# Optimization experiments

Hardware: AMD Instinct MI355X
Metric: run time of the kernel (lower is better)

The kernel has to match this reference:

```python
import jax, jax.numpy as jnp
import numpy as np

N, Q, D = 512, 1024, 256  # num_nodes(=batch), query_len(context len), input_dim


def setup_inputs() -> dict:
    key = jax.random.key(0)
    ks = jax.random.split(key, 7)
    return {
        "query": jax.random.normal(ks[0], (N, 1, D), dtype=jnp.float32),
        "context": jax.random.normal(ks[1], (N, Q, D), dtype=jnp.float32),
        # torch nn.Linear weights are [out_features, in_features]
        "W_in": jax.random.normal(ks[2], (D, D), dtype=jnp.float32) / np.sqrt(D).astype(np.float32),
        "W_out": jax.random.normal(ks[3], (D, 2 * D), dtype=jnp.float32) / np.sqrt(2 * D).astype(np.float32),
        # per-node decay params [num_nodes,1,1]; positive so exp(-ab*dt) decays
        "ae": jax.random.uniform(ks[4], (N, 1, 1), dtype=jnp.float32),
        "ad": jax.random.uniform(ks[5], (N, 1, 1), dtype=jnp.float32),
        "ab": jax.random.uniform(ks[6], (N, 1, 1), dtype=jnp.float32),
        "index": 0,  # stored on self in the original, unused in forward math
    }


def reference(query, context, W_in, W_out, ae, ad, ab, index):
    # general attention: project query
    q = query @ W_in.T                                   # [N,1,D]
    scores = jnp.einsum('bod,bqd->boq', q, context)      # [N,1,Q]
    attention_weights = jax.nn.softmax(scores, axis=-1)  # [N,1,Q]
    ctx_t = jnp.swapaxes(context, 1, 2)                  # [N,D,Q]
    mix = attention_weights * ctx_t                      # [N,D,Q]  (broadcast over D)
    # delta_t = flip(arange(Q)) = [Q-1, ..., 0]
    delta_t = jnp.arange(Q - 1, -1, -1, dtype=jnp.float32)[None, None, :]  # [1,1,Q]
    bt = jnp.exp(-ab * delta_t)                          # [N,1,Q]
    mb = mix * bt                                        # [N,D,Q]
    term_2 = jnp.abs(ae * mb)
    term_3 = jnp.abs(ad * mb)  # |-ad * mix * bt| == |ad * mix * bt|
    mix2 = jnp.tanh(jnp.sum(term_2 + mix - term_3, axis=-1))[:, None, :]  # [N,1,D]
    combined = jnp.concatenate([mix2, q], axis=2)        # [N,1,2D]
    output = jnp.tanh(combined @ W_out.T)                # [N,1,D]
    return output, attention_weights
```

## Files before the change

### kernel.cpp

```cpp
#include <hip/hip_runtime.h>
#include <math.h>

#define N_NODES 512
#define QLEN    1024
#define DIM     256
#define TJ      16
#define LROW    264
#define NT      (QLEN / TJ)

#define AS1 __attribute__((address_space(1)))
#define AS3 __attribute__((address_space(3)))
#define GLD16(gsrc, ldst) \
  __builtin_amdgcn_global_load_lds((AS1 const void*)(gsrc), (AS3 void*)(ldst), 16, 0, 0)

__global__ __launch_bounds__(256, 2) void attn_main_kernel(
    const float* __restrict__ query,
    const float* __restrict__ context,
    const float* __restrict__ W_in,
    const float* __restrict__ ae,
    const float* __restrict__ ad,
    const float* __restrict__ ab,
    float* __restrict__ scores_out,
    float* __restrict__ q_ws,
    float* __restrict__ mix2_ws,
    float* __restrict__ ml_ws)
{
  __shared__ float qs[DIM];
  __shared__ float qv[DIM];
  __shared__ float sc_all[QLEN];
  __shared__ float tile[2][TJ * LROW];

  const int b    = blockIdx.x;
  const int tid  = threadIdx.x;
  const int wave = tid >> 6;
  const int lane = tid & 63;
  const int grp  = tid >> 4;
  const int gl   = tid & 15;

  const float* ctx = context + (size_t)b * QLEN * DIM;

  qs[tid] = query[b * DIM + tid];
  __syncthreads();

  #pragma unroll
  for (int i = 0; i < 4; ++i) {
    const int r = wave + i * 4;
    GLD16(ctx + (size_t)r * DIM + lane * 4, &tile[0][r * LROW]);
  }

  float acc = 0.f;
  {
    const float4* w4 = (const float4*)(W_in + (size_t)tid * DIM);
    #pragma unroll 8
    for (int k = 0; k < DIM / 4; ++k) {
      const float4 wv = w4[k];
      acc += wv.x * qs[4 * k] + wv.y * qs[4 * k + 1] +
             wv.z * qs[4 * k + 2] + wv.w * qs[4 * k + 3];
    }
  }
  qv[tid] = acc;
  q_ws[b * DIM + tid] = acc;

  const float ab_v = ab[b];

  float m = -INFINITY;
  float l = 0.f;
  float accA = 0.f;
  float accB = 0.f;

  for (int t = 0; t < NT; ++t) {
    const int cur = t & 1;

    __syncthreads();

    if (t + 1 < NT) {
      const float* src = ctx + (size_t)(t + 1) * TJ * DIM;
      #pragma unroll
      for (int i = 0; i < 4; ++i) {
        const int r = wave + i * 4;
        GLD16(src + (size_t)r * DIM + lane * 4, &tile[cur ^ 1][r * LROW]);
      }
    }

    {
      const float* trow = &tile[cur][grp * LROW];
      float p = 0.f;
      #pragma unroll
      for (int k = 0; k < TJ; ++k) {
        const int d = gl + 16 * k;
        p += trow[d] * qv[d];
      }
      p += __shfl_xor(p, 1);
      p += __shfl_xor(p, 2);
      p += __shfl_xor(p, 4);
      p += __shfl_xor(p, 8);
      if (gl == 0) sc_all[t * TJ + grp] = p;
    }

    asm volatile("s_waitcnt lgkmcnt(0)\n\ts_barrier" ::: "memory");

    {
      const float* sct = &sc_all[t * TJ];
      float tm = m;
      #pragma unroll
      for (int j = 0; j < TJ; ++j) tm = fmaxf(tm, sct[j]);
      const float rsc = __expf(m - tm);
      m = tm;
      l    *= rsc;
      accA *= rsc;
      accB *= rsc;
      const float* tb  = &tile[cur][tid];
      const float  dt0 = (float)(QLEN - 1 - t * TJ);
      #pragma unroll
      for (int j = 0; j < TJ; ++j) {
        const float w   = __expf(sct[j] - m);
        l += w;
        const float cv  = tb[j * LROW];
        const float btj = __expf(-ab_v * (dt0 - (float)j));
        accA += w * cv;
        accB += w * btj * fabsf(cv);
      }
    }
  }

  const float inv_l = 1.f / l;
  const float cb    = fabsf(ae[b]) - fabsf(ad[b]);
  mix2_ws[b * DIM + tid] = tanhf(accA * inv_l + cb * (accB * inv_l));
  if (tid == 0) { ml_ws[2 * b] = m; ml_ws[2 * b + 1] = l; }

  __syncthreads();
  #pragma unroll
  for (int c = 0; c < 4; ++c)
    scores_out[(size_t)b * QLEN + c * 256 + tid] = sc_all[c * 256 + tid];
}

__global__ __launch_bounds__(256) void out_gemm_kernel(
    const float* __restrict__ W_out,
    const float* __restrict__ q_ws,
    const float* __restrict__ mix2_ws,
    float* __restrict__ out)
{
  __shared__ float comb[2 * DIM];
  const int b = blockIdx.x, tid = threadIdx.x;
  comb[tid]       = mix2_ws[b * DIM + tid];
  comb[DIM + tid] = q_ws[b * DIM + tid];
  __syncthreads();

  const float4* w4 = (const float4*)(W_out + (size_t)tid * 2 * DIM);
  float acc = 0.f;
  #pragma unroll 8
  for (int k = 0; k < (2 * DIM) / 4; ++k) {
    const float4 wv = w4[k];
    acc += wv.x * comb[4 * k] + wv.y * comb[4 * k + 1] +
           wv.z * comb[4 * k + 2] + wv.w * comb[4 * k + 3];
  }
  out[(size_t)b * DIM + tid] = tanhf(acc);
}

__global__ __launch_bounds__(256) void attn_norm_kernel(
    float* __restrict__ scores, const float* __restrict__ ml)
{
  const int i = blockIdx.x * blockDim.x + threadIdx.x;
  const int b = i >> 10;
  const float m = ml[2 * b], l = ml[2 * b + 1];
  scores[i] = __expf(scores[i] - m) / l;
}

extern "C" void kernel_launch(void* const* d_in, const int* in_sizes, int n_in,
                              void* d_out, int out_size, void* d_ws, size_t ws_size,
                              hipStream_t stream) {
  const float* query   = (const float*)d_in[0];
  const float* context = (const float*)d_in[1];
  const float* W_in    = (const float*)d_in[2];
  const float* W_out   = (const float*)d_in[3];
  const float* ae      = (const float*)d_in[4];
  const float* ad      = (const float*)d_in[5];
  const float* ab      = (const float*)d_in[6];

  float* out        = (float*)d_out;
  float* scores_out = (float*)d_out + N_NODES * DIM;

  float* q_ws    = (float*)d_ws;
  float* mix2_ws = q_ws + N_NODES * DIM;
  float* ml_ws   = mix2_ws + N_NODES * DIM;

  hipLaunchKernelGGL(attn_main_kernel, dim3(N_NODES), dim3(256), 0, stream,
                     query, context, W_in, ae, ad, ab,
                     scores_out, q_ws, mix2_ws, ml_ws);
  hipLaunchKernelGGL(out_gemm_kernel, dim3(N_NODES), dim3(256), 0, stream,
                     W_out, q_ws, mix2_ws, out);
  hipLaunchKernelGGL(attn_norm_kernel, dim3((N_NODES * QLEN) / 256), dim3(256), 0, stream,
                     scores_out, ml_ws);
}
```

Measured before the change: 745.9 us.

## Fuse attention, output GEMM and normalization into one barrier-free wave-local kernel

```diff
diff --git a/kernel.cpp b/kernel.cpp
--- a/kernel.cpp
+++ b/kernel.cpp
@@ -7,163 +7,185 @@
 #define TJ      16
 #define LROW    264
 #define NT      (QLEN / TJ)
+#define NBUF    3
 
 #define AS1 __attribute__((address_space(1)))
 #define AS3 __attribute__((address_space(3)))
 #define GLD16(gsrc, ldst) \
   __builtin_amdgcn_global_load_lds((AS1 const void*)(gsrc), (AS3 void*)(ldst), 16, 0, 0)
 
-__global__ __launch_bounds__(256, 2) void attn_main_kernel(
+__global__ __launch_bounds__(256, 2) void rpps_fused_kernel(
     const float* __restrict__ query,
     const float* __restrict__ context,
     const float* __restrict__ W_in,
+    const float* __restrict__ W_out,
     const float* __restrict__ ae,
     const float* __restrict__ ad,
     const float* __restrict__ ab,
-    float* __restrict__ scores_out,
-    float* __restrict__ q_ws,
-    float* __restrict__ mix2_ws,
-    float* __restrict__ ml_ws)
+    float* __restrict__ out,
+    float* __restrict__ scores_out)
 {
   __shared__ float qs[DIM];
   __shared__ float qv[DIM];
-  __shared__ float sc_all[QLEN];
-  __shared__ float tile[2][TJ * LROW];
+  __shared__ float sc[QLEN];
+  __shared__ float comb[2 * DIM];
+  __shared__ float redM[4], redL[4];
+  __shared__ float redA[4][DIM], redB[4][DIM];
+  __shared__ float tile[NBUF][TJ * LROW];
 
   const int b    = blockIdx.x;
   const int tid  = threadIdx.x;
   const int wave = tid >> 6;
   const int lane = tid & 63;
-  const int grp  = tid >> 4;
+  const int wg   = (tid >> 4) & 3;
   const int gl   = tid & 15;
+  const int row  = 4 * wave + wg;
 
   const float* ctx = context + (size_t)b * QLEN * DIM;
 
   qs[tid] = query[b * DIM + tid];
-  __syncthreads();
-
-  #pragma unroll
-  for (int i = 0; i < 4; ++i) {
-    const int r = wave + i * 4;
-    GLD16(ctx + (size_t)r * DIM + lane * 4, &tile[0][r * LROW]);
-  }
-
-  float acc = 0.f;
+
+  #pragma unroll
+  for (int i = 0; i < 4; ++i)
+    GLD16(ctx + (size_t)(4 * wave + i) * DIM + lane * 4,
+          &tile[0][(4 * wave + i) * LROW]);
+  #pragma unroll
+  for (int i = 0; i < 4; ++i)
+    GLD16(ctx + (size_t)(TJ + 4 * wave + i) * DIM + lane * 4,
+          &tile[1][(4 * wave + i) * LROW]);
+
+  asm volatile("s_waitcnt lgkmcnt(0)\n\ts_barrier" ::: "memory");
+
+  float qp = 0.f;
   {
     const float4* w4 = (const float4*)(W_in + (size_t)tid * DIM);
     #pragma unroll 8
     for (int k = 0; k < DIM / 4; ++k) {
       const float4 wv = w4[k];
-      acc += wv.x * qs[4 * k] + wv.y * qs[4 * k + 1] +
-             wv.z * qs[4 * k + 2] + wv.w * qs[4 * k + 3];
-    }
-  }
-  qv[tid] = acc;
-  q_ws[b * DIM + tid] = acc;
+      qp += wv.x * qs[4 * k] + wv.y * qs[4 * k + 1] +
+            wv.z * qs[4 * k + 2] + wv.w * qs[4 * k + 3];
+    }
+  }
+  qv[tid] = qp;
+  asm volatile("s_waitcnt lgkmcnt(0)\n\ts_barrier" ::: "memory");
+
+  float qreg[16];
+  #pragma unroll
+  for (int k = 0; k < 16; ++k) qreg[k] = qv[gl + 16 * k];
 
   const float ab_v = ab[b];
-
-  float m = -INFINITY;
-  float l = 0.f;
-  float accA = 0.f;
-  float accB = 0.f;
-
+  float m_w = -INFINITY, l_w = 0.f;
+  float accA[16], accB[16];
+  #pragma unroll
+  for (int k = 0; k < 16; ++k) { accA[k] = 0.f; accB[k] = 0.f; }
+
+  int slot_c = 0, slot_p = 2;
   for (int t = 0; t < NT; ++t) {
-    const int cur = t & 1;
-
-    __syncthreads();
-
-    if (t + 1 < NT) {
-      const float* src = ctx + (size_t)(t + 1) * TJ * DIM;
+    if (t < NT - 1) asm volatile("s_waitcnt vmcnt(4)" ::: "memory");
+    else            asm volatile("s_waitcnt vmcnt(0)" ::: "memory");
+
+    if (t + 2 < NT) {
+      const float* src = ctx + (size_t)(t + 2) * TJ * DIM;
+      float* dst = &tile[slot_p][0];
       #pragma unroll
-      for (int i = 0; i < 4; ++i) {
-        const int r = wave + i * 4;
-        GLD16(src + (size_t)r * DIM + lane * 4, &tile[cur ^ 1][r * LROW]);
-      }
-    }
-
-    {
-      const float* trow = &tile[cur][grp * LROW];
-      float p = 0.f;
+      for (int i = 0; i < 4; ++i)
+        GLD16(src + (size_t)(4 * wave + i) * DIM + lane * 4,
+              dst + (4 * wave + i) * LROW);
+    }
+
+    const float* trow = &tile[slot_c][row * LROW + gl];
+    float c[16];
+    #pragma unroll
+    for (int k = 0; k < 16; ++k) c[k] = trow[16 * k];
+
+    float s = 0.f;
+    #pragma unroll
+    for (int k = 0; k < 16; ++k) s += c[k] * qreg[k];
+    s += __shfl_xor(s, 1);
+    s += __shfl_xor(s, 2);
+    s += __shfl_xor(s, 4);
+    s += __shfl_xor(s, 8);
+
+    if (gl == 0) sc[t * TJ + row] = s;
+
+    float tm = fmaxf(s, __shfl_xor(s, 16));
+    tm = fmaxf(tm, __shfl_xor(tm, 32));
+
+    if (tm > m_w) {
+      const float rsc = __expf(m_w - tm);
+      m_w = tm;
+      l_w *= rsc;
       #pragma unroll
-      for (int k = 0; k < TJ; ++k) {
-        const int d = gl + 16 * k;
-        p += trow[d] * qv[d];
-      }
-      p += __shfl_xor(p, 1);
-      p += __shfl_xor(p, 2);
-      p += __shfl_xor(p, 4);
-      p += __shfl_xor(p, 8);
-      if (gl == 0) sc_all[t * TJ + grp] = p;
-    }
-
-    asm volatile("s_waitcnt lgkmcnt(0)\n\ts_barrier" ::: "memory");
-
-    {
-      const float* sct = &sc_all[t * TJ];
-      float tm = m;
-      #pragma unroll
-      for (int j = 0; j < TJ; ++j) tm = fmaxf(tm, sct[j]);
-      const float rsc = __expf(m - tm);
-      m = tm;
-      l    *= rsc;
-      accA *= rsc;
-      accB *= rsc;
-      const float* tb  = &tile[cur][tid];
-      const float  dt0 = (float)(QLEN - 1 - t * TJ);
-      #pragma unroll
-      for (int j = 0; j < TJ; ++j) {
-        const float w   = __expf(sct[j] - m);
-        l += w;
-        const float cv  = tb[j * LROW];
-        const float btj = __expf(-ab_v * (dt0 - (float)j));
-        accA += w * cv;
-        accB += w * btj * fabsf(cv);
-      }
-    }
-  }
-
-  const float inv_l = 1.f / l;
-  const float cb    = fabsf(ae[b]) - fabsf(ad[b]);
-  mix2_ws[b * DIM + tid] = tanhf(accA * inv_l + cb * (accB * inv_l));
-  if (tid == 0) { ml_ws[2 * b] = m; ml_ws[2 * b + 1] = l; }
-
+      for (int k = 0; k < 16; ++k) { accA[k] *= rsc; accB[k] *= rsc; }
+    }
+
+    const float w  = __expf(s - m_w);
+    const float bt = __expf(-ab_v * (float)(QLEN - 1 - (t * TJ + row)));
+    const float wb = w * bt;
+    l_w += w;
+    #pragma unroll
+    for (int k = 0; k < 16; ++k) {
+      accA[k] += w * c[k];
+      accB[k] += wb * fabsf(c[k]);
+    }
+
+    if (++slot_c == NBUF) slot_c = 0;
+    if (++slot_p == NBUF) slot_p = 0;
+  }
+
+  #pragma unroll
+  for (int k = 0; k < 16; ++k) {
+    accA[k] += __shfl_xor(accA[k], 16);
+    accA[k] += __shfl_xor(accA[k], 32);
+    accB[k] += __shfl_xor(accB[k], 16);
+    accB[k] += __shfl_xor(accB[k], 32);
+  }
+  l_w += __shfl_xor(l_w, 16);
+  l_w += __shfl_xor(l_w, 32);
+
+  if (lane == 0) { redM[wave] = m_w; redL[wave] = l_w; }
+  if (wg == 0) {
+    #pragma unroll
+    for (int k = 0; k < 16; ++k) {
+      redA[wave][gl + 16 * k] = accA[k];
+      redB[wave][gl + 16 * k] = accB[k];
+    }
+  }
   __syncthreads();
-  #pragma unroll
-  for (int c = 0; c < 4; ++c)
-    scores_out[(size_t)b * QLEN + c * 256 + tid] = sc_all[c * 256 + tid];
-}
-
-__global__ __launch_bounds__(256) void out_gemm_kernel(
-    const float* __restrict__ W_out,
-    const float* __restrict__ q_ws,
-    const float* __restrict__ mix2_ws,
-    float* __restrict__ out)
-{
-  __shared__ float comb[2 * DIM];
-  const int b = blockIdx.x, tid = threadIdx.x;
-  comb[tid]       = mix2_ws[b * DIM + tid];
-  comb[DIM + tid] = q_ws[b * DIM + tid];
+
+  const float M  = fmaxf(fmaxf(redM[0], redM[1]), fmaxf(redM[2], redM[3]));
+  const float e0 = __expf(redM[0] - M), e1 = __expf(redM[1] - M);
+  const float e2 = __expf(redM[2] - M), e3 = __expf(redM[3] - M);
+  const float L  = e0 * redL[0] + e1 * redL[1] + e2 * redL[2] + e3 * redL[3];
+  const float A  = e0 * redA[0][tid] + e1 * redA[1][tid] +
+                   e2 * redA[2][tid] + e3 * redA[3][tid];
+  const float B  = e0 * redB[0][tid] + e1 * redB[1][tid] +
+                   e2 * redB[2][tid] + e3 * redB[3][tid];
+  const float invL = 1.f / L;
+  const float cb   = fabsf(ae[b]) - fabsf(ad[b]);
+
+  comb[tid]       = tanhf((A + cb * B) * invL);
+  comb[DIM + tid] = qp;
+
+  #pragma unroll
+  for (int c2 = 0; c2 < 4; ++c2) {
+    const int j = c2 * 256 + tid;
+    scores_out[(size_t)b * QLEN + j] = __expf(sc[j] - M) * invL;
+  }
+
   __syncthreads();
 
-  const float4* w4 = (const float4*)(W_out + (size_t)tid * 2 * DIM);
-  float acc = 0.f;
-  #pragma unroll 8
-  for (int k = 0; k < (2 * DIM) / 4; ++k) {
-    const float4 wv = w4[k];
-    acc += wv.x * comb[4 * k] + wv.y * comb[4 * k + 1] +
-           wv.z * comb[4 * k + 2] + wv.w * comb[4 * k + 3];
-  }
-  out[(size_t)b * DIM + tid] = tanhf(acc);
-}
-
-__global__ __launch_bounds__(256) void attn_norm_kernel(
-    float* __restrict__ scores, const float* __restrict__ ml)
-{
-  const int i = blockIdx.x * blockDim.x + threadIdx.x;
-  const int b = i >> 10;
-  const float m = ml[2 * b], l = ml[2 * b + 1];
-  scores[i] = __expf(scores[i] - m) / l;
+  float oacc = 0.f;
+  {
+    const float4* wo4 = (const float4*)(W_out + (size_t)tid * 2 * DIM);
+    #pragma unroll 8
+    for (int k = 0; k < (2 * DIM) / 4; ++k) {
+      const float4 wv = wo4[k];
+      oacc += wv.x * comb[4 * k] + wv.y * comb[4 * k + 1] +
+              wv.z * comb[4 * k + 2] + wv.w * comb[4 * k + 3];
+    }
+  }
+  out[(size_t)b * DIM + tid] = tanhf(oacc);
 }
 
 extern "C" void kernel_launch(void* const* d_in, const int* in_sizes, int n_in,
@@ -180,15 +202,6 @@
   float* out        = (float*)d_out;
   float* scores_out = (float*)d_out + N_NODES * DIM;
 
-  float* q_ws    = (float*)d_ws;
-  float* mix2_ws = q_ws + N_NODES * DIM;
-  float* ml_ws   = mix2_ws + N_NODES * DIM;
-
-  hipLaunchKernelGGL(attn_main_kernel, dim3(N_NODES), dim3(256), 0, stream,
-                     query, context, W_in, ae, ad, ab,
-                     scores_out, q_ws, mix2_ws, ml_ws);
-  hipLaunchKernelGGL(out_gemm_kernel, dim3(N_NODES), dim3(256), 0, stream,
-                     W_out, q_ws, mix2_ws, out);
-  hipLaunchKernelGGL(attn_norm_kernel, dim3((N_NODES * QLEN) / 256), dim3(256), 0, stream,
-                     scores_out, ml_ws);
+  hipLaunchKernelGGL(rpps_fused_kernel, dim3(N_NODES), dim3(256), 0, stream,
+                     query, context, W_in, W_out, ae, ad, ab, out, scores_out);
 }
```

After: 724.8 us, median of 2. 2.8% less time.
